# Kernel optimization log

Hardware: AMD Instinct MI355X
Metric: run time of the kernel (lower is better)

Reference implementation:

```python
import jax, jax.numpy as jnp
import numpy as np

D_MODEL = 1024
SEQ_LEN = 2048
NUM_EIGH = 24
BATCH = 4


def _spectral_filters(L, K):
    # Hankel matrix Z[i,j] = 2 / ((i+j)^3 - (i+j)), 1-indexed; top-K eigvecs scaled by sigma^0.25
    t = np.arange(1, L + 1, dtype=np.float64)
    s = t[:, None] + t[None, :]
    Z = 2.0 / (s ** 3 - s)
    sigma, phi = np.linalg.eigh(Z)
    phi_k = phi[:, -K:] * (sigma[-K:] ** 0.25)
    return jnp.asarray(phi_k, dtype=jnp.float32)


def setup_inputs() -> dict:
    key = jax.random.key(0)
    k1, k2, k3 = jax.random.split(key, 3)
    std = 1.0 / np.sqrt(D_MODEL)
    return {
        "x": jax.random.normal(k1, (BATCH, SEQ_LEN, D_MODEL), dtype=jnp.float32),
        "M_inputs": jax.random.normal(k2, (D_MODEL, D_MODEL), dtype=jnp.float32) * std,
        "M_filters": jax.random.normal(k3, (NUM_EIGH, D_MODEL), dtype=jnp.float32) * std,
        "phi": _spectral_filters(SEQ_LEN, NUM_EIGH),
    }


def _convolve_approx(u, v, n):
    # u: [B, L, D] inputs (already projected); v: [L, D] per-channel causal filters.
    # Dual-branch causal FFT convolution:
    #   plus[b,t,d]  = sum_{s<=t} v[s,d] * u[b,t-s,d]
    #   minus[b,t,d] = (-1)^t * sum_{s<=t} v[s,d] * (-1)^{t-s} u[b,t-s,d]
    B, L, D = u.shape
    sgn = jnp.where(jnp.arange(L) % 2 == 0, 1.0, -1.0).astype(u.dtype)[None, :, None]  # [1,L,1]
    V = jnp.fft.rfft(v, n=n, axis=0)                     # [F, D] complex
    U = jnp.stack([u, u * sgn], axis=-1)                 # [B, L, D, 2]
    Uf = jnp.fft.rfft(U, n=n, axis=1)                    # [B, F, D, 2]
    conv = jnp.fft.irfft(V[None, :, :, None] * Uf, n=n, axis=1)[:, :L]  # [B, L, D, 2]
    return conv[..., 0], conv[..., 1] * sgn


def reference(x, M_inputs, M_filters, phi):
    L = x.shape[1]
    n = 1 << int(np.ceil(np.log2(2 * L - 1)))  # next pow2 of 2L-1 (static)
    x_proj = x @ M_inputs                       # [B, L, D]
    phi_proj = phi[:L] @ M_filters              # [L, D]
    spectral_plus, spectral_minus = _convolve_approx(x_proj, phi_proj, n)
    return spectral_plus + spectral_minus
```

## Files before the change

kernel.cpp:

```cpp
#include <hip/hip_runtime.h>
#include <stdint.h>

#define D_MODEL 1024
#define SEQ 2048
#define HALF 1024
#define K_EIG 24
#define GUARD4 24
#define K4 128
#define K4P (GUARD4 + K4)
#define WE_JP4 72

typedef __attribute__((ext_vector_type(8))) short bf16x8;
typedef __attribute__((ext_vector_type(4))) float f32x4;
typedef _Float16 f16;
typedef _Float16 f16x2 __attribute__((ext_vector_type(2)));
typedef unsigned int uint;

#define GAS __attribute__((address_space(1)))
#define LAS __attribute__((address_space(3)))

static __device__ __forceinline__ unsigned short f2bf(float f) {
  union { float f; uint32_t u; } v; v.f = f;
  uint32_t u = v.u;
  u += 0x7FFFu + ((u >> 16) & 1u);
  return (unsigned short)(u >> 16);
}

static __device__ __forceinline__ float dot2(uint w2, uint u2, float c) {
  return __builtin_amdgcn_fdot2(__builtin_bit_cast(f16x2, w2),
                                __builtin_bit_cast(f16x2, u2), c, false);
}

static __device__ __forceinline__ uint pkrtz(float lo, float hi) {
  return __builtin_bit_cast(uint, __builtin_amdgcn_cvt_pkrtz(lo, hi));
}

static __device__ __forceinline__ uint pkbf(float lo, float hi) {
  return (uint)f2bf(lo) | ((uint)f2bf(hi) << 16);
}

__global__ __launch_bounds__(256) void k_prep(const float* __restrict__ Mi,
                                              const float* __restrict__ phi,
                                              const float* __restrict__ Mf,
                                              uint4* __restrict__ u4,
                                              unsigned short* __restrict__ Mt,
                                              uint4* __restrict__ we4) {
  __shared__ float smem[1056];
  const int blk = (int)blockIdx.x;
  const int tidx = threadIdx.x;

  if (blk < 768) {
    int r = blk / 96;
    int idx = (blk - r * 96) * 256 + tidx;
    u4[(size_t)r * (K4P * 1024) + idx] = make_uint4(0u, 0u, 0u, 0u);
    return;
  }
  if (blk < 1792) {
    int bidx = blk - 768;
    int n0 = (bidx & 31) * 32, k0 = (bidx >> 5) * 32;
    float (*tile)[33] = (float(*)[33])smem;
    int tx = tidx & 31, ty = tidx >> 5;
    #pragma unroll
    for (int r = 0; r < 32; r += 8)
      tile[ty + r][tx] = Mi[(size_t)(k0 + ty + r) * D_MODEL + n0 + tx];
    __syncthreads();
    #pragma unroll
    for (int r = 0; r < 32; r += 8)
      Mt[(size_t)(n0 + ty + r) * D_MODEL + k0 + tx] = f2bf(tile[tx][ty + r]);
    return;
  }
  {
    int bidx = blk - 1792;
    int jp4 = bidx % 72;
    int d = (bidx / 72) * 256 + tidx;
    if (jp4 >= 64) {
      we4[(size_t)jp4 * D_MODEL + d] = make_uint4(0u, 0u, 0u, 0u);
      return;
    }
    float (*ph)[K_EIG] = (float(*)[K_EIG])smem;
    if (tidx < 8 * K_EIG) {
      int s = tidx / K_EIG, k = tidx - s * K_EIG;
      ph[s][k] = phi[(size_t)(16 * jp4 + 2 * s) * K_EIG + k];
    }
    __syncthreads();
    float s[8] = {};
    #pragma unroll
    for (int k = 0; k < K_EIG; ++k) {
      float mv = Mf[(size_t)k * D_MODEL + d];
      #pragma unroll
      for (int j = 0; j < 8; ++j) s[j] = fmaf(ph[j][k], mv, s[j]);
    }
    uint4 o;
    o.x = pkrtz(2.f * s[0], 2.f * s[1]);
    o.y = pkrtz(2.f * s[2], 2.f * s[3]);
    o.z = pkrtz(2.f * s[4], 2.f * s[5]);
    o.w = pkrtz(2.f * s[6], 2.f * s[7]);
    we4[(size_t)jp4 * D_MODEL + d] = o;
  }
}

__global__ __launch_bounds__(256) void k_gemm(const float* __restrict__ X,
                                              const unsigned short* __restrict__ Bt,
                                              uint* __restrict__ Ug) {
  __shared__ float Asf[3][128 * 32];
  __shared__ unsigned short Bs[3][128 * 32];
  const int bid = (int)blockIdx.x;
  const int swz = (bid & 7) * 64 + (bid >> 3);
  const int m0 = (swz >> 3) * 128;
  const int n0 = (swz & 7) * 128;
  const int tid = threadIdx.x;
  const int lane = tid & 63;
  const int wave = tid >> 6;
  const int wm = wave >> 1, wn = wave & 1;
  const int qo = lane >> 4;

  const int a_row = lane >> 3;
  const int a_chunk = (lane & 7) ^ a_row;
  const int b_row = lane >> 2;
  const int b_chunk = (lane & 3) ^ (b_row & 3);

#define GSTAGE(buf, k0v)                                                                  \
  {                                                                                       \
    float* abase = &Asf[buf][0];                                                          \
    unsigned short* bbase = &Bs[buf][0];                                                  \
    _Pragma("unroll") for (int c = 0; c < 4; ++c) {                                       \
      int rbase = wave * 32 + c * 8;                                                      \
      const float* srcA = X + (size_t)(m0 + rbase + a_row) * 1024 + (k0v) + a_chunk * 4;  \
      __builtin_amdgcn_global_load_lds((const GAS void*)srcA,                             \
                                       (LAS void*)(abase + rbase * 32), 16, 0, 0);        \
    }                                                                                     \
    _Pragma("unroll") for (int c = 0; c < 2; ++c) {                                       \
      int rbase = wave * 32 + c * 16;                                                     \
      const unsigned short* srcB = Bt + (size_t)(n0 + rbase + b_row) * 1024 + (k0v) + b_chunk * 8; \
      __builtin_amdgcn_global_load_lds((const GAS void*)srcB,                             \
                                       (LAS void*)(bbase + rbase * 32), 16, 0, 0);        \
    }                                                                                     \
  }

  f32x4 acc[4][4] = {};

  GSTAGE(0, 0);
  GSTAGE(1, 32);

  int cur = 0;
  int nx2 = 2;
#pragma unroll 1
  for (int t = 0; t < 32; ++t) {
    if (t < 31) {
      asm volatile("s_waitcnt vmcnt(6)" ::: "memory");
    } else {
      asm volatile("s_waitcnt vmcnt(0)" ::: "memory");
    }
    __builtin_amdgcn_s_barrier();
    asm volatile("" ::: "memory");
    if (t < 30) GSTAGE(nx2, (t + 2) * 32);

    bf16x8 a[4], b[4];
    const float* Acur = &Asf[cur][0];
    const unsigned short* Bcur = &Bs[cur][0];
    #pragma unroll
    for (int mt = 0; mt < 4; ++mt) {
      int m = wm * 64 + mt * 16 + (lane & 15);
      const float* base = Acur + m * 32;
      int s0 = (2 * qo) ^ (lane & 7);
      int s1 = s0 ^ 1;
      float4 f0 = *(const float4*)(base + s0 * 4);
      float4 f1 = *(const float4*)(base + s1 * 4);
      uint4 pk;
      pk.x = pkbf(f0.x, f0.y); pk.y = pkbf(f0.z, f0.w);
      pk.z = pkbf(f1.x, f1.y); pk.w = pkbf(f1.z, f1.w);
      a[mt] = __builtin_bit_cast(bf16x8, pk);
    }
    #pragma unroll
    for (int nt = 0; nt < 4; ++nt) {
      int n = wn * 64 + nt * 16 + (lane & 15);
      int sb = qo ^ (lane & 3);
      b[nt] = *(const bf16x8*)(Bcur + n * 32 + sb * 8);
    }
    #pragma unroll
    for (int mt = 0; mt < 4; ++mt)
      #pragma unroll
      for (int nt = 0; nt < 4; ++nt)
        acc[mt][nt] = __builtin_amdgcn_mfma_f32_16x16x32_bf16(a[mt], b[nt], acc[mt][nt], 0, 0, 0);

    cur = (cur == 2) ? 0 : cur + 1;
    nx2 = (nx2 == 2) ? 0 : nx2 + 1;
  }
#undef GSTAGE

  const int crow = (lane >> 4) * 4;
  const int ccol = lane & 15;
  #pragma unroll
  for (int mt = 0; mt < 4; ++mt) {
    int m = m0 + wm * 64 + mt * 16 + crow;
    int b_ = m >> 11;
    int t0 = m & 2047;
    int r_e = b_ << 1;
    int k4 = t0 >> 4;
    int dwo = (t0 >> 2) & 3;
    size_t base_e = ((size_t)(r_e * K4P + GUARD4 + k4) * 1024) * 4 + dwo;
    size_t base_o = ((size_t)((r_e + 1) * K4P + GUARD4 + k4) * 1024) * 4 + dwo;
    #pragma unroll
    for (int nt = 0; nt < 4; ++nt) {
      int n = n0 + wn * 64 + nt * 16 + ccol;
      Ug[base_e + (size_t)n * 4] = pkrtz(acc[mt][nt][0], acc[mt][nt][2]);
      Ug[base_o + (size_t)n * 4] = pkrtz(acc[mt][nt][1], acc[mt][nt][3]);
    }
  }
}

__global__ __launch_bounds__(512, 8) void k_conv(const uint4* __restrict__ u4,
                                                 const uint4* __restrict__ we4,
                                                 float* __restrict__ out) {
  __shared__ uint4 u_r[32 * 64];
  const int flat = blockIdx.x;
  const int dt = flat & 15;
  const int r  = (flat >> 4) & 7;
  const int a  = 7 - (flat >> 7);
  const int d0 = dt * 64;
  const int tid = threadIdx.x;
  const int dl = tid & 63;
  const int ig = tid >> 6;

  const uint4* ub = u4 + ((size_t)r * K4P + GUARD4) * 1024 + d0;
  const uint4* wb = we4 + d0 + dl;
  const int b_ = r >> 1, p = r & 1;

#define STAGEU(k40)                                                                     \
  {                                                                                     \
    int k4e = (k40) + ig;                                                               \
    const uint4* src = ub + (long long)k4e * 1024 + dl;                                 \
    __builtin_amdgcn_global_load_lds((const GAS void*)src,                              \
                                     (LAS void*)(u_r + (k4e & 31) * 64), 16, 0, 0);     \
  }

#define DOTS(kb_, wv0, wv1)                                                             \
  {                                                                                     \
    const int kb = (kb_);                                                               \
    uint4 v0 = u_r[((kb + 0) & 31) * 64 + dl];                                          \
    uint4 v1 = u_r[((kb + 1) & 31) * 64 + dl];                                          \
    uint4 v2 = u_r[((kb + 2) & 31) * 64 + dl];                                          \
    uint4 v3 = u_r[((kb + 3) & 31) * 64 + dl];                                          \
    uint P[16];                                                                         \
    P[0] = v0.x; P[1] = v0.y; P[2] = v0.z; P[3] = v0.w;                                 \
    P[4] = v1.x; P[5] = v1.y; P[6] = v1.z; P[7] = v1.w;                                 \
    P[8] = v2.x; P[9] = v2.y; P[10] = v2.z; P[11] = v2.w;                               \
    P[12] = v3.x; P[13] = v3.y; P[14] = v3.z; P[15] = v3.w;                             \
    uint W[8];                                                                          \
    W[0] = (wv0).x; W[1] = (wv0).y; W[2] = (wv0).z; W[3] = (wv0).w;                     \
    W[4] = (wv1).x; W[5] = (wv1).y; W[6] = (wv1).z; W[7] = (wv1).w;                     \
    uint WS[8];                                                                         \
    _Pragma("unroll") for (int q = 0; q < 8; ++q)                                       \
      WS[q] = __builtin_amdgcn_alignbit(W[q], W[q], 16);                                \
    uint pe[15];                                                                        \
    _Pragma("unroll") for (int j = 0; j < 15; ++j)                                      \
      pe[j] = __builtin_amdgcn_perm(P[j + 1], P[j], 0x03020504u);                       \
    _Pragma("unroll") for (int q = 0; q < 8; ++q) {                                     \
      _Pragma("unroll") for (int h = 0; h < 8; ++h) {                                   \
        acc[2 * h]     = dot2(W[q],  pe[7 - q + h], acc[2 * h]);                        \
        acc[2 * h + 1] = dot2(WS[q], P[8 - q + h],  acc[2 * h + 1]);                    \
      }                                                                                 \
    }                                                                                   \
  }

  const int i0 = a * 128;
  const int ibase = i0 + ig * 16;
  const int niter = (2 * a + 2) < 8 ? (2 * a + 2) : 8;

  STAGEU(16 * a - 8); STAGEU(16 * a); STAGEU(16 * a + 8);
  __syncthreads();

  float acc[16];
#pragma unroll
  for (int o = 0; o < 16; ++o) acc[o] = 0.f;

  uint4 wA0 = wb[0], wA1 = wb[1024];
  uint4 wB0, wB1;

#pragma unroll 1
  for (int c = 0; c < niter; ++c) {
    STAGEU(16 * a - 8 * c - 16);
    const int kbase = 16 * a + 2 * ig - 8 * c - 2;
    wB0 = wb[(size_t)(8 * c + 2) * 1024]; wB1 = wb[(size_t)(8 * c + 3) * 1024];
    DOTS(kbase - 0, wA0, wA1);
    wA0 = wb[(size_t)(8 * c + 4) * 1024]; wA1 = wb[(size_t)(8 * c + 5) * 1024];
    DOTS(kbase - 2, wB0, wB1);
    wB0 = wb[(size_t)(8 * c + 6) * 1024]; wB1 = wb[(size_t)(8 * c + 7) * 1024];
    DOTS(kbase - 4, wA0, wA1);
    wA0 = wb[(size_t)(8 * c + 8) * 1024]; wA1 = wb[(size_t)(8 * c + 9) * 1024];
    DOTS(kbase - 6, wB0, wB1);
    __syncthreads();
  }

#pragma unroll
  for (int o = 0; o < 16; ++o)
    out[((size_t)b_ * SEQ + 2 * (ibase + o) + p) * D_MODEL + d0 + dl] = acc[o];
#undef STAGEU
#undef DOTS
}

extern "C" void kernel_launch(void* const* d_in, const int* in_sizes, int n_in,
                              void* d_out, int out_size, void* d_ws, size_t ws_size,
                              hipStream_t stream) {
  const float* x   = (const float*)d_in[0];
  const float* Mi  = (const float*)d_in[1];
  const float* Mf  = (const float*)d_in[2];
  const float* phi = (const float*)d_in[3];
  float* out = (float*)d_out;

  unsigned short* Mt = (unsigned short*)d_out;

  char* ws = (char*)d_ws;
  uint4* we4 = (uint4*)(ws);
  uint4* u4  = (uint4*)(ws + (2u << 20));

  hipLaunchKernelGGL(k_prep, dim3(2080), dim3(256), 0, stream, Mi, phi, Mf, u4, Mt, we4);
  hipLaunchKernelGGL(k_gemm, dim3(512), dim3(256), 0, stream, x, Mt, (uint*)u4);
  hipLaunchKernelGGL(k_conv, dim3(1024), dim3(512), 0, stream, u4, we4, out);
}
```

Before: 118.9 us.

## Pre-convert X to bf16 in prep kernel and simplify GEMM to double buffering

Adds a pass in the prep kernel that converts the whole fp32 input X to bf16 and stores it in the output buffer. The GEMM then loads bf16 A tiles directly, with no per-iteration fp32-to-bf16 packing, and switches from a three-stage buffer with vmcnt waits to a two-stage buffer using __syncthreads. This halves A-tile LDS and global traffic inside the GEMM and removes conversion ALU work. In exchange it adds an extra full read and write of X (32MB read, 16MB write) and a shallower prefetch pipeline.

```diff
diff --git a/kernel.cpp b/kernel.cpp
--- a/kernel.cpp
+++ b/kernel.cpp
@@ -35,28 +35,35 @@
   return __builtin_bit_cast(uint, __builtin_amdgcn_cvt_pkrtz(lo, hi));
 }
 
-static __device__ __forceinline__ uint pkbf(float lo, float hi) {
-  return (uint)f2bf(lo) | ((uint)f2bf(hi) << 16);
-}
-
-__global__ __launch_bounds__(256) void k_prep(const float* __restrict__ Mi,
+__global__ __launch_bounds__(256) void k_prep(const float* __restrict__ X,
+                                              const float* __restrict__ Mi,
                                               const float* __restrict__ phi,
                                               const float* __restrict__ Mf,
                                               uint4* __restrict__ u4,
+                                              unsigned short* __restrict__ x_bf,
                                               unsigned short* __restrict__ Mt,
                                               uint4* __restrict__ we4) {
   __shared__ float smem[1056];
   const int blk = (int)blockIdx.x;
   const int tidx = threadIdx.x;
 
-  if (blk < 768) {
-    int r = blk / 96;
-    int idx = (blk - r * 96) * 256 + tidx;
+  if (blk < 8192) {
+    int idx = blk * 256 + tidx;
+    float4 v = ((const float4*)X)[idx];
+    ushort4 o;
+    o.x = f2bf(v.x); o.y = f2bf(v.y); o.z = f2bf(v.z); o.w = f2bf(v.w);
+    ((ushort4*)x_bf)[idx] = o;
+    return;
+  }
+  if (blk < 8960) {
+    int b2 = blk - 8192;
+    int r = b2 / 96;
+    int idx = (b2 - r * 96) * 256 + tidx;
     u4[(size_t)r * (K4P * 1024) + idx] = make_uint4(0u, 0u, 0u, 0u);
     return;
   }
-  if (blk < 1792) {
-    int bidx = blk - 768;
+  if (blk < 9984) {
+    int bidx = blk - 8960;
     int n0 = (bidx & 31) * 32, k0 = (bidx >> 5) * 32;
     float (*tile)[33] = (float(*)[33])smem;
     int tx = tidx & 31, ty = tidx >> 5;
@@ -70,7 +77,7 @@
     return;
   }
   {
-    int bidx = blk - 1792;
+    int bidx = blk - 9984;
     int jp4 = bidx % 72;
     int d = (bidx / 72) * 256 + tidx;
     if (jp4 >= 64) {
@@ -99,11 +106,11 @@
   }
 }
 
-__global__ __launch_bounds__(256) void k_gemm(const float* __restrict__ X,
+__global__ __launch_bounds__(256) void k_gemm(const unsigned short* __restrict__ A,
                                               const unsigned short* __restrict__ Bt,
                                               uint* __restrict__ Ug) {
-  __shared__ float Asf[3][128 * 32];
-  __shared__ unsigned short Bs[3][128 * 32];
+  __shared__ unsigned short As[2][128 * 32];
+  __shared__ unsigned short Bs[2][128 * 32];
   const int bid = (int)blockIdx.x;
   const int swz = (bid & 7) * 64 + (bid >> 3);
   const int m0 = (swz >> 3) * 128;
@@ -114,77 +121,47 @@
   const int wm = wave >> 1, wn = wave & 1;
   const int qo = lane >> 4;
 
-  const int a_row = lane >> 3;
-  const int a_chunk = (lane & 7) ^ a_row;
-  const int b_row = lane >> 2;
-  const int b_chunk = (lane & 3) ^ (b_row & 3);
+  const int row_ = lane >> 2;
+  const int chunk_ = (lane & 3) ^ (row_ & 3);
 
 #define GSTAGE(buf, k0v)                                                                  \
   {                                                                                       \
-    float* abase = &Asf[buf][0];                                                          \
-    unsigned short* bbase = &Bs[buf][0];                                                  \
-    _Pragma("unroll") for (int c = 0; c < 4; ++c) {                                       \
-      int rbase = wave * 32 + c * 8;                                                      \
-      const float* srcA = X + (size_t)(m0 + rbase + a_row) * 1024 + (k0v) + a_chunk * 4;  \
-      __builtin_amdgcn_global_load_lds((const GAS void*)srcA,                             \
-                                       (LAS void*)(abase + rbase * 32), 16, 0, 0);        \
-    }                                                                                     \
     _Pragma("unroll") for (int c = 0; c < 2; ++c) {                                       \
       int rbase = wave * 32 + c * 16;                                                     \
-      const unsigned short* srcB = Bt + (size_t)(n0 + rbase + b_row) * 1024 + (k0v) + b_chunk * 8; \
+      const unsigned short* srcA = A + (size_t)(m0 + rbase + row_) * 1024 + (k0v) + chunk_ * 8; \
+      __builtin_amdgcn_global_load_lds((const GAS void*)srcA,                             \
+                                       (LAS void*)(&As[buf][0] + rbase * 32), 16, 0, 0);  \
+      const unsigned short* srcB = Bt + (size_t)(n0 + rbase + row_) * 1024 + (k0v) + chunk_ * 8; \
       __builtin_amdgcn_global_load_lds((const GAS void*)srcB,                             \
-                                       (LAS void*)(bbase + rbase * 32), 16, 0, 0);        \
+                                       (LAS void*)(&Bs[buf][0] + rbase * 32), 16, 0, 0);  \
     }                                                                                     \
   }
 
   f32x4 acc[4][4] = {};
 
   GSTAGE(0, 0);
-  GSTAGE(1, 32);
-
-  int cur = 0;
-  int nx2 = 2;
+  __syncthreads();
+
 #pragma unroll 1
   for (int t = 0; t < 32; ++t) {
-    if (t < 31) {
-      asm volatile("s_waitcnt vmcnt(6)" ::: "memory");
-    } else {
-      asm volatile("s_waitcnt vmcnt(0)" ::: "memory");
-    }
-    __builtin_amdgcn_s_barrier();
-    asm volatile("" ::: "memory");
-    if (t < 30) GSTAGE(nx2, (t + 2) * 32);
-
+    const int cur = t & 1;
+    if (t < 31) GSTAGE(cur ^ 1, (t + 1) * 32);
+
+    const int sa = qo ^ (lane & 3);
     bf16x8 a[4], b[4];
-    const float* Acur = &Asf[cur][0];
-    const unsigned short* Bcur = &Bs[cur][0];
-    #pragma unroll
-    for (int mt = 0; mt < 4; ++mt) {
-      int m = wm * 64 + mt * 16 + (lane & 15);
-      const float* base = Acur + m * 32;
-      int s0 = (2 * qo) ^ (lane & 7);
-      int s1 = s0 ^ 1;
-      float4 f0 = *(const float4*)(base + s0 * 4);
-      float4 f1 = *(const float4*)(base + s1 * 4);
-      uint4 pk;
-      pk.x = pkbf(f0.x, f0.y); pk.y = pkbf(f0.z, f0.w);
-      pk.z = pkbf(f1.x, f1.y); pk.w = pkbf(f1.z, f1.w);
-      a[mt] = __builtin_bit_cast(bf16x8, pk);
-    }
-    #pragma unroll
-    for (int nt = 0; nt < 4; ++nt) {
-      int n = wn * 64 + nt * 16 + (lane & 15);
-      int sb = qo ^ (lane & 3);
-      b[nt] = *(const bf16x8*)(Bcur + n * 32 + sb * 8);
-    }
+    #pragma unroll
+    for (int mt = 0; mt < 4; ++mt)
+      a[mt] = *(const bf16x8*)(&As[cur][0] + (wm * 64 + mt * 16 + (lane & 15)) * 32 + sa * 8);
+    #pragma unroll
+    for (int nt = 0; nt < 4; ++nt)
+      b[nt] = *(const bf16x8*)(&Bs[cur][0] + (wn * 64 + nt * 16 + (lane & 15)) * 32 + sa * 8);
     #pragma unroll
     for (int mt = 0; mt < 4; ++mt)
       #pragma unroll
       for (int nt = 0; nt < 4; ++nt)
         acc[mt][nt] = __builtin_amdgcn_mfma_f32_16x16x32_bf16(a[mt], b[nt], acc[mt][nt], 0, 0, 0);
 
-    cur = (cur == 2) ? 0 : cur + 1;
-    nx2 = (nx2 == 2) ? 0 : nx2 + 1;
+    __syncthreads();
   }
 #undef GSTAGE
 
@@ -308,13 +285,14 @@
   const float* phi = (const float*)d_in[3];
   float* out = (float*)d_out;
 
-  unsigned short* Mt = (unsigned short*)d_out;
+  unsigned short* x_bf = (unsigned short*)d_out;
+  unsigned short* Mt   = (unsigned short*)((char*)d_out + (16u << 20));
 
   char* ws = (char*)d_ws;
   uint4* we4 = (uint4*)(ws);
   uint4* u4  = (uint4*)(ws + (2u << 20));
 
-  hipLaunchKernelGGL(k_prep, dim3(2080), dim3(256), 0, stream, Mi, phi, Mf, u4, Mt, we4);
-  hipLaunchKernelGGL(k_gemm, dim3(512), dim3(256), 0, stream, x, Mt, (uint*)u4);
+  hipLaunchKernelGGL(k_prep, dim3(10272), dim3(256), 0, stream, x, Mi, phi, Mf, u4, x_bf, Mt, we4);
+  hipLaunchKernelGGL(k_gemm, dim3(512), dim3(256), 0, stream, x_bf, Mt, (uint*)u4);
   hipLaunchKernelGGL(k_conv, dim3(1024), dim3(512), 0, stream, u4, we4, out);
 }
```

Measured after the change: 114.4 us. 3.9% less time.
